# Optimization experiments

Measured on AMD Instinct MI355X. Metric: run time of the kernel, lower is better.

## Reference

```python
import jax, jax.numpy as jnp
import numpy as np

D = 1024          # node_vec_size = 16 heads * 64 head_size
HEADS = 16
DH = 64
HID = 4096        # TFM_HIDDEN_SIZE
L = 12            # TFM_NUM_LAYERS
NC = 256          # num concepts present (WMG2_MAX_CONCEPTS)
CSZ = 128         # WMG2_CONCEPT_SIZE
MAX_AGE = 256     # WMG2_MAX_AGE
AGE_V = MAX_AGE + 2  # 258
OBS = 2048
OUT = 512         # WMG2_OUTPUT_LAYER_SIZE
SCALE = 0.02


def setup_inputs() -> dict:
    key = jax.random.key(0)
    ks = iter(jax.random.split(key, 40))
    rn = lambda shape: jax.random.normal(next(ks), shape, dtype=jnp.float32) * SCALE
    inp = {
        'observation': jax.random.normal(next(ks), (OBS,), dtype=jnp.float32),
        'concepts': jax.random.normal(next(ks), (NC, CSZ), dtype=jnp.float32),
        'W_core': rn((D, OBS)), 'b_core': jnp.zeros((D,), jnp.float32),
        'W_cemb': rn((D, CSZ)), 'b_cemb': jnp.zeros((D,), jnp.float32),
        'W_age': rn((D, AGE_V)), 'b_age': jnp.zeros((D,), jnp.float32),
        'Wq': rn((L, D, D)), 'bq': jnp.zeros((L, D), jnp.float32),
        'Wk': rn((L, D, D)), 'bk': jnp.zeros((L, D), jnp.float32),
        'Wv': rn((L, D, D)), 'bv': jnp.zeros((L, D), jnp.float32),
        'Wo': rn((L, D, D)), 'bo': jnp.zeros((L, D), jnp.float32),
        'ln1_g': jnp.ones((L, D), jnp.float32), 'ln1_b': jnp.zeros((L, D), jnp.float32),
        'W1': rn((L, HID, D)), 'b1': jnp.zeros((L, HID), jnp.float32),
        'W2': rn((L, D, HID)), 'b2': jnp.zeros((L, D), jnp.float32),
        'ln2_g': jnp.ones((L, D), jnp.float32), 'ln2_b': jnp.zeros((L, D), jnp.float32),
        'W_concept': rn((CSZ, D)), 'b_concept': jnp.zeros((CSZ,), jnp.float32),
        'W_out': rn((OUT, D)), 'b_out': jnp.zeros((OUT,), jnp.float32),
    }
    return inp


def _layernorm(x, g, b, eps=1e-5):
    m = jnp.mean(x, axis=-1, keepdims=True)
    v = jnp.var(x, axis=-1, keepdims=True)
    return (x - m) * jax.lax.rsqrt(v + eps) * g + b


def _forward(observation, concepts, W_core, b_core, W_cemb, b_cemb, W_age, b_age,
             Wq, bq, Wk, bk, Wv, bv, Wo, bo, ln1_g, ln1_b, W1, b1, W2, b2,
             ln2_g, ln2_b, W_concept, b_concept, W_out, b_out):
    # --- embed observation node ---
    x0 = observation @ W_core.T + b_core                      # [D]
    # --- embed concept nodes, vectorized age embedding ---
    ages = jnp.arange(NC)
    oh = jax.nn.one_hot(jnp.minimum(ages, AGE_V - 1), AGE_V, dtype=jnp.float32)
    oh = oh.at[:, -1].set(ages.astype(jnp.float32) / MAX_AGE)  # age[-1] = age/MAX_AGE
    age_emb = oh @ W_age.T + b_age                             # [NC, D]
    xc = concepts @ W_cemb.T + b_cemb + age_emb                # [NC, D]
    x = jnp.concatenate([x0[None, :], xc], axis=0)             # [S, D], S = 1+NC

    # --- transformer (post-LN encoder), scan over layers ---
    def layer(h, p):
        wq, bq_, wk, bk_, wv, bv_, wo, bo_, g1, be1, w1, b1_, w2, b2_, g2, be2 = p
        S = h.shape[0]
        q = (h @ wq.T + bq_).reshape(S, HEADS, DH)
        k = (h @ wk.T + bk_).reshape(S, HEADS, DH)
        v = (h @ wv.T + bv_).reshape(S, HEADS, DH)
        scores = jnp.einsum('qhd,khd->hqk', q, k) / jnp.sqrt(jnp.float32(DH))
        attn = jax.nn.softmax(scores, axis=-1)
        o = jnp.einsum('hqk,khd->qhd', attn, v).reshape(S, D)
        h = _layernorm(h + (o @ wo.T + bo_), g1, be1)
        f = jax.nn.relu(h @ w1.T + b1_) @ w2.T + b2_
        h = _layernorm(h + f, g2, be2)
        return h, None

    x, _ = jax.lax.scan(layer, x, (Wq, bq, Wk, bk, Wv, bv, Wo, bo,
                                   ln1_g, ln1_b, W1, b1, W2, b2, ln2_g, ln2_b))
    tfm_out = x[0]                                             # [D] (node 0)
    new_concept = jnp.tanh(tfm_out @ W_concept.T + b_concept)  # [CSZ]
    output = jax.nn.relu(tfm_out @ W_out.T + b_out)[None, :]   # [1, OUT]
    return output, new_concept


def reference(observation, concepts, W_core, b_core, W_cemb, b_cemb, W_age, b_age,
              Wq, bq, Wk, bk, Wv, bv, Wo, bo, ln1_g, ln1_b, W1, b1, W2, b2,
              ln2_g, ln2_b, W_concept, b_concept, W_out, b_out):
    return _forward(observation, concepts, W_core, b_core, W_cemb, b_cemb, W_age, b_age,
                    Wq, bq, Wk, bk, Wv, bv, Wo, bo, ln1_g, ln1_b, W1, b1, W2, b2,
                    ln2_g, ln2_b, W_concept, b_concept, W_out, b_out)
```

## Files before the change

kernel.cpp:

```cpp
#include <hip/hip_runtime.h>
#include <hip/hip_bf16.h>
#include <cmath>

constexpr int D     = 1024;
constexpr int HEADS = 16;
constexpr int DH    = 64;
constexpr int HID   = 4096;
constexpr int NL    = 12;
constexpr int NC    = 256;
constexpr int CSZ   = 128;
constexpr int AGE_V = 258;
constexpr int OBS   = 2048;
constexpr int OUTN  = 512;
constexpr int S     = 257;
constexpr int SP    = 288;

typedef __attribute__((ext_vector_type(8))) short bf16x8v;
typedef __attribute__((ext_vector_type(4))) short short4v;
typedef __attribute__((ext_vector_type(4))) float f32x4;

__device__ __forceinline__ short bfc(float x) {
    __hip_bfloat16 h = __float2bfloat16(x);
    return __builtin_bit_cast(short, h);
}
__device__ __forceinline__ void st_bf16x4(short* p, float4 v) {
    short4v s;
    s.x = bfc(v.x); s.y = bfc(v.y); s.z = bfc(v.z); s.w = bfc(v.w);
    *(short4v*)p = s;
}

constexpr int BM = 96, BN = 32, BK = 64, LDT = 72;

template<int EPI>
__device__ __forceinline__ void gemm_core(const short* __restrict__ A,
                                          const float* __restrict__ B,
                                          const float* __restrict__ bias,
                                          void* __restrict__ Cp,
                                          int K, int N, int kbeg, int klen) {
    __shared__ __align__(16) short As[BM * LDT];
    __shared__ __align__(16) short Bs[BN * LDT];
    const int t  = threadIdx.x;
    const int m0 = blockIdx.y * BM;
    const int n0 = blockIdx.x * BN;
    const int ar = t >> 3;
    const int ac = (t & 7) * 8;
    const short* Ab = A + (size_t)(m0 + ar) * K + kbeg + ac;
    const int sr = t >> 4;
    const int sc = (t & 15) * 4;
    const float* Bb = B + (size_t)(n0 + sr) * K + kbeg + sc;

    const int lane = t & 63, wave = t >> 6;
    const int wm = wave >> 1, wn = wave & 1;
    const int fr = lane & 15, quad = lane >> 4;
    const short* Abase = &As[(wm * 48 + fr) * LDT + quad * 8];
    const short* Bbase = &Bs[(wn * 16 + fr) * LDT + quad * 8];

    f32x4 acc[3] = {};

    bf16x8v areg[3];
    float4  breg[2];
    #pragma unroll
    for (int p = 0; p < 3; ++p)
        areg[p] = *(const bf16x8v*)(Ab + (size_t)(p * 32) * K);
    #pragma unroll
    for (int p = 0; p < 2; ++p)
        breg[p] = *(const float4*)(Bb + (size_t)(p * 16) * K);

    for (int k0 = 0; k0 < klen; k0 += BK) {
        __syncthreads();
        #pragma unroll
        for (int p = 0; p < 3; ++p)
            *(bf16x8v*)&As[(p * 32 + ar) * LDT + ac] = areg[p];
        #pragma unroll
        for (int p = 0; p < 2; ++p)
            st_bf16x4(&Bs[(p * 16 + sr) * LDT + sc], breg[p]);
        __syncthreads();
        if (k0 + BK < klen) {
            #pragma unroll
            for (int p = 0; p < 3; ++p)
                areg[p] = *(const bf16x8v*)(Ab + (size_t)(p * 32) * K + (k0 + BK));
            #pragma unroll
            for (int p = 0; p < 2; ++p)
                breg[p] = *(const float4*)(Bb + (size_t)(p * 16) * K + (k0 + BK));
        }
        #pragma unroll
        for (int kt = 0; kt < 2; ++kt) {
            bf16x8v af[3], bf;
            #pragma unroll
            for (int mt = 0; mt < 3; ++mt)
                af[mt] = *(const bf16x8v*)(Abase + mt * 16 * LDT + kt * 32);
            bf = *(const bf16x8v*)(Bbase + kt * 32);
            #pragma unroll
            for (int mt = 0; mt < 3; ++mt)
                acc[mt] = __builtin_amdgcn_mfma_f32_16x16x32_bf16(
                    af[mt], bf, acc[mt], 0, 0, 0);
        }
    }

    #pragma unroll
    for (int mt = 0; mt < 3; ++mt) {
        const int m = m0 + wm * 48 + mt * 16 + quad * 4;
        const int n = n0 + wn * 16 + fr;
        if (EPI == 2) {
            float* C = (float*)Cp;
            #pragma unroll
            for (int r = 0; r < 4; ++r)
                atomicAdd(&C[(size_t)(m + r) * N + n], acc[mt][r]);
        } else if (EPI == 1) {
            short* C = (short*)Cp;
            const float bvv = bias[n];
            #pragma unroll
            for (int r = 0; r < 4; ++r)
                C[(size_t)(m + r) * N + n] = bfc(fmaxf(acc[mt][r] + bvv, 0.f));
        } else {
            float* C = (float*)Cp;
            const float bvv = bias[n];
            #pragma unroll
            for (int r = 0; r < 4; ++r)
                C[(size_t)(m + r) * N + n] = acc[mt][r] + bvv;
        }
    }
}

template<int EPI>
__global__ __launch_bounds__(256, 3)
void gemm_splitk(const short* __restrict__ A, const float* __restrict__ B,
                 const float* __restrict__ bias, void* __restrict__ C,
                 int K, int N, int klen) {
    gemm_core<EPI>(A, B, bias, C, K, N, blockIdx.z * klen, klen);
}

struct QKVArgs {
    const float* B[3];
    const float* bias[3];
    float* C[3];
};

__global__ __launch_bounds__(256, 3)
void gemm_qkv(const short* __restrict__ A, QKVArgs args, int K, int N) {
    const int z = blockIdx.z;
    gemm_core<0>(A, args.B[z], args.bias[z], args.C[z], K, N, 0, K);
}

constexpr int QB = 8, KT = 32, NT = 9;

__global__ __launch_bounds__(512)
void attn_kernel(const float* __restrict__ Q, const float* __restrict__ Km,
                 const float* __restrict__ V, short* __restrict__ O) {
    __shared__ float Ks[KT * 66];
    __shared__ float Vs[KT * 64];
    __shared__ float pw[QB][NT * KT];
    const int h = blockIdx.y;
    const int t = threadIdx.x;
    const int wq = t >> 6, lane = t & 63;
    const int q = blockIdx.x * QB + wq;
    const bool qok = q < S;
    const int k32 = lane & 31, dh2 = lane >> 5;

    float qr[32];
    #pragma unroll
    for (int i = 0; i < 32; ++i)
        qr[i] = qok ? Q[(size_t)q * D + h * DH + dh2 * 32 + i] : 0.f;

    float s[NT];
    for (int tile = 0; tile < NT; ++tile) {
        const int kk0 = tile * KT;
        __syncthreads();
        #pragma unroll
        for (int p = 0; p < 2; ++p) {
            const int idx = t + p * 512;
            const int kr = idx >> 5, c2 = (idx & 31) * 2;
            const int kg = kk0 + kr;
            float2 v = make_float2(0.f, 0.f);
            if (kg < S) v = *(const float2*)&Km[(size_t)kg * D + h * DH + c2];
            *(float2*)&Ks[kr * 66 + c2] = v;
        }
        __syncthreads();
        float dot = 0.f;
        const float* kp = &Ks[k32 * 66 + dh2 * 32];
        #pragma unroll
        for (int i = 0; i < 32; ++i) dot = fmaf(qr[i], kp[i], dot);
        dot += __shfl_xor(dot, 32, 64);
        s[tile] = (kk0 + k32 < S) ? dot * 0.125f : -1e30f;
    }
    float mx = -1e30f;
    #pragma unroll
    for (int j = 0; j < NT; ++j) mx = fmaxf(mx, s[j]);
    #pragma unroll
    for (int off = 32; off; off >>= 1) mx = fmaxf(mx, __shfl_xor(mx, off, 64));
    float sum = 0.f;
    #pragma unroll
    for (int j = 0; j < NT; ++j) {
        const float e = __expf(s[j] - mx);
        s[j] = e;
        sum += e;
    }
    #pragma unroll
    for (int off = 32; off; off >>= 1) sum += __shfl_xor(sum, off, 64);
    sum *= 0.5f;
    const float inv = 1.f / sum;
    if (qok && dh2 == 0) {
        #pragma unroll
        for (int j = 0; j < NT; ++j) pw[wq][j * KT + k32] = s[j] * inv;
    }
    float acc = 0.f;
    for (int tile = 0; tile < NT; ++tile) {
        const int kk0 = tile * KT;
        __syncthreads();
        {
            const int kr = t >> 4, c4 = (t & 15) * 4;
            const int kg = kk0 + kr;
            float4 v = make_float4(0.f, 0.f, 0.f, 0.f);
            if (kg < S) v = *(const float4*)&V[(size_t)kg * D + h * DH + c4];
            *(float4*)&Vs[kr * 64 + c4] = v;
        }
        __syncthreads();
        if (qok) {
            const float* pwp = &pw[wq][kk0];
            #pragma unroll
            for (int k = 0; k < KT; ++k)
                acc = fmaf(pwp[k], Vs[k * 64 + lane], acc);
        }
    }
    if (qok) O[(size_t)q * D + h * DH + lane] = bfc(acc);
}

__global__ __launch_bounds__(256)
void embed_obs_kernel(const float* __restrict__ obs, const float* __restrict__ Wc,
                      const float* __restrict__ bc, const float* __restrict__ bo0,
                      float* __restrict__ H, short* __restrict__ HB,
                      float* __restrict__ T) {
    const int d = blockIdx.x;
    const int t = threadIdx.x;
    const float4* w4 = (const float4*)&Wc[(size_t)d * OBS];
    const float4* o4 = (const float4*)obs;
    float acc = 0.f;
    #pragma unroll
    for (int i = t; i < OBS / 4; i += 256) {
        const float4 a = o4[i];
        const float4 b = w4[i];
        acc = fmaf(a.x, b.x, acc); acc = fmaf(a.y, b.y, acc);
        acc = fmaf(a.z, b.z, acc); acc = fmaf(a.w, b.w, acc);
    }
    __shared__ float red[256];
    red[t] = acc;
    __syncthreads();
    for (int off = 128; off; off >>= 1) {
        if (t < off) red[t] += red[t + off];
        __syncthreads();
    }
    if (t == 0) {
        const float v = red[0] + bc[d];
        H[d] = v;
        HB[d] = bfc(v);
        T[d] = v + bo0[d];
    }
}

__global__ __launch_bounds__(256)
void embed_concepts_kernel(const float* __restrict__ concepts, const float* __restrict__ Wce,
                           const float* __restrict__ bce, const float* __restrict__ Wa,
                           const float* __restrict__ ba, const float* __restrict__ bo0,
                           float* __restrict__ H, short* __restrict__ HB,
                           short* __restrict__ ATT, float* __restrict__ T) {
    const int row = blockIdx.x + 1;
    const int d = blockIdx.y * 256 + threadIdx.x;
    if (row > NC) {
        H[(size_t)row * D + d] = 0.f;
        HB[(size_t)row * D + d] = 0;
        ATT[(size_t)row * D + d] = 0;
        T[(size_t)row * D + d] = bo0[d];
        return;
    }
    const int i = row - 1;
    __shared__ __align__(16) float cs[CSZ];
    if (threadIdx.x < CSZ) cs[threadIdx.x] = concepts[(size_t)i * CSZ + threadIdx.x];
    __syncthreads();
    const float4* w4 = (const float4*)&Wce[(size_t)d * CSZ];
    const float4* c4 = (const float4*)cs;
    float acc = 0.f;
    #pragma unroll
    for (int c = 0; c < CSZ / 4; ++c) {
        const float4 a = c4[c];
        const float4 b = w4[c];
        acc = fmaf(a.x, b.x, acc); acc = fmaf(a.y, b.y, acc);
        acc = fmaf(a.z, b.z, acc); acc = fmaf(a.w, b.w, acc);
    }
    const float age = Wa[(size_t)d * AGE_V + i] +
                      ((float)i / 256.f) * Wa[(size_t)d * AGE_V + (AGE_V - 1)];
    const float v = acc + bce[d] + ba[d] + age;
    H[(size_t)row * D + d] = v;
    HB[(size_t)row * D + d] = bfc(v);
    T[(size_t)row * D + d] = v + bo0[d];
}

__global__ __launch_bounds__(256)
void ln_kernel(const float* __restrict__ X, const float* __restrict__ g,
               const float* __restrict__ b, float* __restrict__ Y,
               short* __restrict__ Yb,
               float* __restrict__ Tinit, const float* __restrict__ nbias) {
    const int r = blockIdx.x;
    const int t = threadIdx.x;
    const float* x = X + (size_t)r * D;
    float sm = 0.f, ss = 0.f;
    float v[4];
    #pragma unroll
    for (int j = 0; j < 4; ++j) {
        const float u = x[t + j * 256];
        v[j] = u;
        sm += u;
        ss = fmaf(u, u, ss);
    }
    __shared__ float r1[256], r2[256];
    r1[t] = sm; r2[t] = ss;
    __syncthreads();
    for (int off = 128; off; off >>= 1) {
        if (t < off) { r1[t] += r1[t + off]; r2[t] += r2[t + off]; }
        __syncthreads();
    }
    const float m   = r1[0] * (1.f / D);
    const float var = r2[0] * (1.f / D) - m * m;
    const float rs  = rsqrtf(var + 1e-5f);
    #pragma unroll
    for (int j = 0; j < 4; ++j) {
        const int idx = t + j * 256;
        const float y = (v[j] - m) * rs * g[idx] + b[idx];
        Y[(size_t)r * D + idx] = y;
        Yb[(size_t)r * D + idx] = bfc(y);
        if (Tinit) Tinit[(size_t)r * D + idx] = y + nbias[idx];
    }
}

__global__ __launch_bounds__(256)
void head_kernel(const float* __restrict__ H, const float* __restrict__ Wout,
                 const float* __restrict__ bout, const float* __restrict__ Wcon,
                 const float* __restrict__ bcon, float* __restrict__ out) {
    const int j = blockIdx.x;
    const int t = threadIdx.x;
    const float* w = (j < OUTN) ? &Wout[(size_t)j * D] : &Wcon[(size_t)(j - OUTN) * D];
    const float4* w4 = (const float4*)w;
    const float4* h4 = (const float4*)H;
    const float4 a = h4[t];
    const float4 b = w4[t];
    float acc = a.x * b.x + a.y * b.y + a.z * b.z + a.w * b.w;
    __shared__ float red[256];
    red[t] = acc;
    __syncthreads();
    for (int off = 128; off; off >>= 1) {
        if (t < off) red[t] += red[t + off];
        __syncthreads();
    }
    if (t == 0) {
        const float v = red[0] + ((j < OUTN) ? bout[j] : bcon[j - OUTN]);
        out[j] = (j < OUTN) ? fmaxf(v, 0.f) : tanhf(v);
    }
}

extern "C" void kernel_launch(void* const* d_in, const int* in_sizes, int n_in,
                              void* d_out, int out_size, void* d_ws, size_t ws_size,
                              hipStream_t stream) {
    (void)in_sizes; (void)n_in; (void)out_size; (void)ws_size;
    const float* obs     = (const float*)d_in[0];
    const float* concepts= (const float*)d_in[1];
    const float* W_core  = (const float*)d_in[2];
    const float* b_core  = (const float*)d_in[3];
    const float* W_cemb  = (const float*)d_in[4];
    const float* b_cemb  = (const float*)d_in[5];
    const float* W_age   = (const float*)d_in[6];
    const float* b_age   = (const float*)d_in[7];
    const float* Wq      = (const float*)d_in[8];
    const float* bq      = (const float*)d_in[9];
    const float* Wk      = (const float*)d_in[10];
    const float* bk      = (const float*)d_in[11];
    const float* Wv      = (const float*)d_in[12];
    const float* bv      = (const float*)d_in[13];
    const float* Wo      = (const float*)d_in[14];
    const float* bo      = (const float*)d_in[15];
    const float* ln1g    = (const float*)d_in[16];
    const float* ln1b    = (const float*)d_in[17];
    const float* W1      = (const float*)d_in[18];
    const float* b1      = (const float*)d_in[19];
    const float* W2      = (const float*)d_in[20];
    const float* b2      = (const float*)d_in[21];
    const float* ln2g    = (const float*)d_in[22];
    const float* ln2b    = (const float*)d_in[23];
    const float* W_con   = (const float*)d_in[24];
    const float* b_con   = (const float*)d_in[25];
    const float* W_out   = (const float*)d_in[26];
    const float* b_out   = (const float*)d_in[27];
    float* outp = (float*)d_out;

    float* ws   = (float*)d_ws;
    float* h    = ws;
    float* tmpA = h    + (size_t)SP * D;
    float* tmpB = tmpA + (size_t)SP * D;
    float* qb   = tmpB + (size_t)SP * D;
    float* kb   = qb   + (size_t)SP * D;
    float* vb   = kb   + (size_t)SP * D;
    short* hb   = (short*)(vb + (size_t)SP * D);
    short* att  = hb  + (size_t)SP * D;
    short* mid  = att + (size_t)SP * D;

    embed_obs_kernel<<<dim3(D), 256, 0, stream>>>(obs, W_core, b_core, bo, h, hb, tmpA);
    embed_concepts_kernel<<<dim3(SP - 1, D / 256), 256, 0, stream>>>(
        concepts, W_cemb, b_cemb, W_age, b_age, bo, h, hb, att, tmpA);

    for (int l = 0; l < NL; ++l) {
        QKVArgs qa;
        qa.B[0] = Wq + (size_t)l * D * D;  qa.bias[0] = bq + (size_t)l * D;  qa.C[0] = qb;
        qa.B[1] = Wk + (size_t)l * D * D;  qa.bias[1] = bk + (size_t)l * D;  qa.C[1] = kb;
        qa.B[2] = Wv + (size_t)l * D * D;  qa.bias[2] = bv + (size_t)l * D;  qa.C[2] = vb;
        gemm_qkv<<<dim3(D / BN, SP / BM, 3), 256, 0, stream>>>(hb, qa, D, D);
        attn_kernel<<<dim3((S + QB - 1) / QB, HEADS), 512, 0, stream>>>(qb, kb, vb, att);
        gemm_splitk<2><<<dim3(D / BN, SP / BM, 4), 256, 0, stream>>>(
            att, Wo + (size_t)l * D * D, nullptr, tmpA, D, D, 256);
        ln_kernel<<<dim3(S), 256, 0, stream>>>(tmpA, ln1g + (size_t)l * D,
                                               ln1b + (size_t)l * D, h, hb,
                                               tmpB, b2 + (size_t)l * D);
        gemm_splitk<1><<<dim3(HID / BN, SP / BM, 1), 256, 0, stream>>>(
            hb, W1 + (size_t)l * HID * D, b1 + (size_t)l * HID, mid, D, HID, D);
        gemm_splitk<2><<<dim3(D / BN, SP / BM, 8), 256, 0, stream>>>(
            mid, W2 + (size_t)l * D * HID, nullptr, tmpB, HID, D, 512);
        float* ti = (l + 1 < NL) ? tmpA : nullptr;
        const float* nb = (l + 1 < NL) ? (bo + (size_t)(l + 1) * D) : nullptr;
        ln_kernel<<<dim3(S), 256, 0, stream>>>(tmpB, ln2g + (size_t)l * D,
                                               ln2b + (size_t)l * D, h, hb, ti, nb);
    }
    head_kernel<<<dim3(OUTN + CSZ), 256, 0, stream>>>(h, W_out, b_out, W_con, b_con, outp);
}
```

Before: 1.541 ms.

## Fuse whole transformer forward into one cooperative persistent megakernel with grid syncs

Replaces the sequence of roughly a hundred separate kernel launches with a single cooperative persistent kernel. Each stage (embeddings, QKV GEMM, attention, output projection, layernorms, FFN GEMMs, head) becomes a device job loop over a grid-stride schedule, separated by grid.sync, and all stages share one static shared-memory buffer. This is meant to remove per-launch overhead and inter-kernel gaps. Attention is re-tiled to 4 queries per 256-thread block, and the W2 split-K factor drops from 8 to 4 inside the megakernel. The trade-offs are grid-wide barrier costs, fewer blocks per GEMM stage, and register limits from the shared launch bounds. A non-cooperative multi-launch fallback is kept for when the cooperative launch fails.

```diff
diff --git a/kernel.cpp b/kernel.cpp
--- a/kernel.cpp
+++ b/kernel.cpp
@@ -1,6 +1,9 @@
 #include <hip/hip_runtime.h>
+#include <hip/hip_cooperative_groups.h>
 #include <hip/hip_bf16.h>
 #include <cmath>
+
+namespace cg = cooperative_groups;
 
 constexpr int D     = 1024;
 constexpr int HEADS = 16;
@@ -30,24 +33,23 @@
 }
 
 constexpr int BM = 96, BN = 32, BK = 64, LDT = 72;
+constexpr int SMEM_BYTES = 21504;
 
 template<int EPI>
-__device__ __forceinline__ void gemm_core(const short* __restrict__ A,
-                                          const float* __restrict__ B,
-                                          const float* __restrict__ bias,
-                                          void* __restrict__ Cp,
-                                          int K, int N, int kbeg, int klen) {
-    __shared__ __align__(16) short As[BM * LDT];
-    __shared__ __align__(16) short Bs[BN * LDT];
-    const int t  = threadIdx.x;
-    const int m0 = blockIdx.y * BM;
-    const int n0 = blockIdx.x * BN;
+__device__ __forceinline__ void gemm_job(char* smraw, const short* __restrict__ A,
+                                         const float* __restrict__ Bm,
+                                         const float* __restrict__ bias,
+                                         void* __restrict__ Cp,
+                                         int K, int N, int kbeg, int klen,
+                                         int m0, int n0, int t) {
+    short* As = (short*)smraw;
+    short* Bs = (short*)(smraw + 13824);
     const int ar = t >> 3;
     const int ac = (t & 7) * 8;
     const short* Ab = A + (size_t)(m0 + ar) * K + kbeg + ac;
     const int sr = t >> 4;
     const int sc = (t & 15) * 4;
-    const float* Bb = B + (size_t)(n0 + sr) * K + kbeg + sc;
+    const float* Bb = Bm + (size_t)(n0 + sr) * K + kbeg + sc;
 
     const int lane = t & 63, wave = t >> 6;
     const int wm = wave >> 1, wn = wave & 1;
@@ -56,7 +58,6 @@
     const short* Bbase = &Bs[(wn * 16 + fr) * LDT + quad * 8];
 
     f32x4 acc[3] = {};
-
     bf16x8v areg[3];
     float4  breg[2];
     #pragma unroll
@@ -85,15 +86,15 @@
         }
         #pragma unroll
         for (int kt = 0; kt < 2; ++kt) {
-            bf16x8v af[3], bf;
+            bf16x8v af[3], bfv;
             #pragma unroll
             for (int mt = 0; mt < 3; ++mt)
                 af[mt] = *(const bf16x8v*)(Abase + mt * 16 * LDT + kt * 32);
-            bf = *(const bf16x8v*)(Bbase + kt * 32);
+            bfv = *(const bf16x8v*)(Bbase + kt * 32);
             #pragma unroll
             for (int mt = 0; mt < 3; ++mt)
                 acc[mt] = __builtin_amdgcn_mfma_f32_16x16x32_bf16(
-                    af[mt], bf, acc[mt], 0, 0, 0);
+                    af[mt], bfv, acc[mt], 0, 0, 0);
         }
     }
 
@@ -122,38 +123,18 @@
     }
 }
 
-template<int EPI>
-__global__ __launch_bounds__(256, 3)
-void gemm_splitk(const short* __restrict__ A, const float* __restrict__ B,
-                 const float* __restrict__ bias, void* __restrict__ C,
-                 int K, int N, int klen) {
-    gemm_core<EPI>(A, B, bias, C, K, N, blockIdx.z * klen, klen);
-}
-
-struct QKVArgs {
-    const float* B[3];
-    const float* bias[3];
-    float* C[3];
-};
-
-__global__ __launch_bounds__(256, 3)
-void gemm_qkv(const short* __restrict__ A, QKVArgs args, int K, int N) {
-    const int z = blockIdx.z;
-    gemm_core<0>(A, args.B[z], args.bias[z], args.C[z], K, N, 0, K);
-}
-
-constexpr int QB = 8, KT = 32, NT = 9;
-
-__global__ __launch_bounds__(512)
-void attn_kernel(const float* __restrict__ Q, const float* __restrict__ Km,
-                 const float* __restrict__ V, short* __restrict__ O) {
-    __shared__ float Ks[KT * 66];
-    __shared__ float Vs[KT * 64];
-    __shared__ float pw[QB][NT * KT];
-    const int h = blockIdx.y;
-    const int t = threadIdx.x;
+constexpr int KT = 32, NT = 9;
+
+__device__ __forceinline__ void attn_job(char* smraw, const float* __restrict__ Q,
+                                         const float* __restrict__ Km,
+                                         const float* __restrict__ V,
+                                         short* __restrict__ O,
+                                         int h, int qt, int t) {
+    float* Ks = (float*)smraw;
+    float* Vs = (float*)(smraw + 8448);
+    float* pw = (float*)(smraw + 8448 + 8192);
     const int wq = t >> 6, lane = t & 63;
-    const int q = blockIdx.x * QB + wq;
+    const int q = qt * 4 + wq;
     const bool qok = q < S;
     const int k32 = lane & 31, dh2 = lane >> 5;
 
@@ -167,8 +148,8 @@
         const int kk0 = tile * KT;
         __syncthreads();
         #pragma unroll
-        for (int p = 0; p < 2; ++p) {
-            const int idx = t + p * 512;
+        for (int p = 0; p < 4; ++p) {
+            const int idx = t + p * 256;
             const int kr = idx >> 5, c2 = (idx & 31) * 2;
             const int kg = kk0 + kr;
             float2 v = make_float2(0.f, 0.f);
@@ -201,14 +182,16 @@
     const float inv = 1.f / sum;
     if (qok && dh2 == 0) {
         #pragma unroll
-        for (int j = 0; j < NT; ++j) pw[wq][j * KT + k32] = s[j] * inv;
+        for (int j = 0; j < NT; ++j) pw[wq * 288 + j * KT + k32] = s[j] * inv;
     }
     float acc = 0.f;
     for (int tile = 0; tile < NT; ++tile) {
         const int kk0 = tile * KT;
         __syncthreads();
-        {
-            const int kr = t >> 4, c4 = (t & 15) * 4;
+        #pragma unroll
+        for (int p = 0; p < 2; ++p) {
+            const int idx = t + p * 256;
+            const int kr = idx >> 4, c4 = (idx & 15) * 4;
             const int kg = kk0 + kr;
             float4 v = make_float4(0.f, 0.f, 0.f, 0.f);
             if (kg < S) v = *(const float4*)&V[(size_t)kg * D + h * DH + c4];
@@ -216,7 +199,7 @@
         }
         __syncthreads();
         if (qok) {
-            const float* pwp = &pw[wq][kk0];
+            const float* pwp = &pw[wq * 288 + kk0];
             #pragma unroll
             for (int k = 0; k < KT; ++k)
                 acc = fmaf(pwp[k], Vs[k * 64 + lane], acc);
@@ -225,13 +208,13 @@
     if (qok) O[(size_t)q * D + h * DH + lane] = bfc(acc);
 }
 
-__global__ __launch_bounds__(256)
-void embed_obs_kernel(const float* __restrict__ obs, const float* __restrict__ Wc,
-                      const float* __restrict__ bc, const float* __restrict__ bo0,
-                      float* __restrict__ H, short* __restrict__ HB,
-                      float* __restrict__ T) {
-    const int d = blockIdx.x;
-    const int t = threadIdx.x;
+__device__ __forceinline__ void embed_obs_job(char* smraw, const float* __restrict__ obs,
+                                              const float* __restrict__ Wc,
+                                              const float* __restrict__ bc,
+                                              const float* __restrict__ bo0,
+                                              float* __restrict__ H, short* __restrict__ HB,
+                                              float* __restrict__ T, int d, int t) {
+    float* red = (float*)smraw;
     const float4* w4 = (const float4*)&Wc[(size_t)d * OBS];
     const float4* o4 = (const float4*)obs;
     float acc = 0.f;
@@ -242,7 +225,7 @@
         acc = fmaf(a.x, b.x, acc); acc = fmaf(a.y, b.y, acc);
         acc = fmaf(a.z, b.z, acc); acc = fmaf(a.w, b.w, acc);
     }
-    __shared__ float red[256];
+    __syncthreads();
     red[t] = acc;
     __syncthreads();
     for (int off = 128; off; off >>= 1) {
@@ -257,14 +240,17 @@
     }
 }
 
-__global__ __launch_bounds__(256)
-void embed_concepts_kernel(const float* __restrict__ concepts, const float* __restrict__ Wce,
-                           const float* __restrict__ bce, const float* __restrict__ Wa,
-                           const float* __restrict__ ba, const float* __restrict__ bo0,
-                           float* __restrict__ H, short* __restrict__ HB,
-                           short* __restrict__ ATT, float* __restrict__ T) {
-    const int row = blockIdx.x + 1;
-    const int d = blockIdx.y * 256 + threadIdx.x;
+__device__ __forceinline__ void embed_cpt_job(char* smraw, const float* __restrict__ concepts,
+                                              const float* __restrict__ Wce,
+                                              const float* __restrict__ bce,
+                                              const float* __restrict__ Wa,
+                                              const float* __restrict__ ba,
+                                              const float* __restrict__ bo0,
+                                              float* __restrict__ H, short* __restrict__ HB,
+                                              short* __restrict__ ATT, float* __restrict__ T,
+                                              int j, int t) {
+    const int row = (j % 287) + 1;
+    const int d = (j / 287) * 256 + t;
     if (row > NC) {
         H[(size_t)row * D + d] = 0.f;
         HB[(size_t)row * D + d] = 0;
@@ -272,9 +258,10 @@
         T[(size_t)row * D + d] = bo0[d];
         return;
     }
+    float* cs = (float*)smraw;
     const int i = row - 1;
-    __shared__ __align__(16) float cs[CSZ];
-    if (threadIdx.x < CSZ) cs[threadIdx.x] = concepts[(size_t)i * CSZ + threadIdx.x];
+    __syncthreads();
+    if (t < CSZ) cs[t] = concepts[(size_t)i * CSZ + t];
     __syncthreads();
     const float4* w4 = (const float4*)&Wce[(size_t)d * CSZ];
     const float4* c4 = (const float4*)cs;
@@ -294,13 +281,13 @@
     T[(size_t)row * D + d] = v + bo0[d];
 }
 
-__global__ __launch_bounds__(256)
-void ln_kernel(const float* __restrict__ X, const float* __restrict__ g,
-               const float* __restrict__ b, float* __restrict__ Y,
-               short* __restrict__ Yb,
-               float* __restrict__ Tinit, const float* __restrict__ nbias) {
-    const int r = blockIdx.x;
-    const int t = threadIdx.x;
+__device__ __forceinline__ void ln_job(char* smraw, const float* __restrict__ X,
+                                       const float* __restrict__ g, const float* __restrict__ b,
+                                       float* __restrict__ Y, short* __restrict__ Yb,
+                                       float* __restrict__ Ti, const float* __restrict__ nbias,
+                                       int r, int t) {
+    float* r1 = (float*)smraw;
+    float* r2 = r1 + 256;
     const float* x = X + (size_t)r * D;
     float sm = 0.f, ss = 0.f;
     float v[4];
@@ -311,7 +298,7 @@
         sm += u;
         ss = fmaf(u, u, ss);
     }
-    __shared__ float r1[256], r2[256];
+    __syncthreads();
     r1[t] = sm; r2[t] = ss;
     __syncthreads();
     for (int off = 128; off; off >>= 1) {
@@ -327,23 +314,24 @@
         const float y = (v[j] - m) * rs * g[idx] + b[idx];
         Y[(size_t)r * D + idx] = y;
         Yb[(size_t)r * D + idx] = bfc(y);
-        if (Tinit) Tinit[(size_t)r * D + idx] = y + nbias[idx];
-    }
-}
-
-__global__ __launch_bounds__(256)
-void head_kernel(const float* __restrict__ H, const float* __restrict__ Wout,
-                 const float* __restrict__ bout, const float* __restrict__ Wcon,
-                 const float* __restrict__ bcon, float* __restrict__ out) {
-    const int j = blockIdx.x;
-    const int t = threadIdx.x;
+        if (Ti) Ti[(size_t)r * D + idx] = y + nbias[idx];
+    }
+}
+
+__device__ __forceinline__ void head_job(char* smraw, const float* __restrict__ H,
+                                         const float* __restrict__ Wout,
+                                         const float* __restrict__ bout,
+                                         const float* __restrict__ Wcon,
+                                         const float* __restrict__ bcon,
+                                         float* __restrict__ out, int j, int t) {
+    float* red = (float*)smraw;
     const float* w = (j < OUTN) ? &Wout[(size_t)j * D] : &Wcon[(size_t)(j - OUTN) * D];
     const float4* w4 = (const float4*)w;
     const float4* h4 = (const float4*)H;
     const float4 a = h4[t];
     const float4 b = w4[t];
     float acc = a.x * b.x + a.y * b.y + a.z * b.z + a.w * b.w;
-    __shared__ float red[256];
+    __syncthreads();
     red[t] = acc;
     __syncthreads();
     for (int off = 128; off; off >>= 1) {
@@ -354,6 +342,117 @@
         const float v = red[0] + ((j < OUTN) ? bout[j] : bcon[j - OUTN]);
         out[j] = (j < OUTN) ? fmaxf(v, 0.f) : tanhf(v);
     }
+}
+
+struct MP {
+    const float *obs, *concepts, *W_core, *b_core, *W_cemb, *b_cemb, *W_age, *b_age;
+    const float *Wq, *bq, *Wk, *bk, *Wv, *bv, *Wo, *bo;
+    const float *ln1g, *ln1b, *W1, *b1, *W2, *b2, *ln2g, *ln2b;
+    const float *W_con, *b_con, *W_out, *b_out;
+    float *outp;
+    float *h, *tmpA, *tmpB, *qb, *kb, *vb;
+    short *hb, *att, *mid;
+};
+
+__global__ __launch_bounds__(256, 2)
+void mega(MP p) {
+    __shared__ __align__(16) char smraw[SMEM_BYTES];
+    cg::grid_group grid = cg::this_grid();
+    const int t = threadIdx.x;
+    const int nb = gridDim.x, bid = blockIdx.x;
+
+    for (int j = bid; j < D; j += nb)
+        embed_obs_job(smraw, p.obs, p.W_core, p.b_core, p.bo, p.h, p.hb, p.tmpA, j, t);
+    for (int j = bid; j < 287 * 4; j += nb)
+        embed_cpt_job(smraw, p.concepts, p.W_cemb, p.b_cemb, p.W_age, p.b_age, p.bo,
+                      p.h, p.hb, p.att, p.tmpA, j, t);
+    grid.sync();
+
+    for (int l = 0; l < NL; ++l) {
+        const size_t lo = (size_t)l * D * D;
+        for (int j = bid; j < 288; j += nb) {
+            const int n = j & 31, m = (j >> 5) % 3, z = j / 96;
+            const float *Bm, *bs;
+            float* Cm;
+            if (z == 0)      { Bm = p.Wq + lo; bs = p.bq + (size_t)l * D; Cm = p.qb; }
+            else if (z == 1) { Bm = p.Wk + lo; bs = p.bk + (size_t)l * D; Cm = p.kb; }
+            else             { Bm = p.Wv + lo; bs = p.bv + (size_t)l * D; Cm = p.vb; }
+            gemm_job<0>(smraw, p.hb, Bm, bs, Cm, D, D, 0, D, m * 96, n * 32, t);
+        }
+        grid.sync();
+        for (int j = bid; j < 65 * 16; j += nb)
+            attn_job(smraw, p.qb, p.kb, p.vb, p.att, j / 65, j % 65, t);
+        grid.sync();
+        for (int j = bid; j < 384; j += nb) {
+            const int n = j & 31, m = (j >> 5) % 3, z = j / 96;
+            gemm_job<2>(smraw, p.att, p.Wo + lo, nullptr, p.tmpA, D, D,
+                        z * 256, 256, m * 96, n * 32, t);
+        }
+        grid.sync();
+        for (int j = bid; j < S; j += nb)
+            ln_job(smraw, p.tmpA, p.ln1g + (size_t)l * D, p.ln1b + (size_t)l * D,
+                   p.h, p.hb, p.tmpB, p.b2 + (size_t)l * D, j, t);
+        grid.sync();
+        for (int j = bid; j < 384; j += nb) {
+            const int n = j % 128, m = j / 128;
+            gemm_job<1>(smraw, p.hb, p.W1 + (size_t)l * HID * D, p.b1 + (size_t)l * HID,
+                        p.mid, D, HID, 0, D, m * 96, n * 32, t);
+        }
+        grid.sync();
+        for (int j = bid; j < 384; j += nb) {
+            const int n = j & 31, m = (j >> 5) % 3, z = j / 96;
+            gemm_job<2>(smraw, p.mid, p.W2 + (size_t)l * D * HID, nullptr, p.tmpB,
+                        HID, D, z * 1024, 1024, m * 96, n * 32, t);
+        }
+        grid.sync();
+        float* ti = (l + 1 < NL) ? p.tmpA : nullptr;
+        const float* nbias = (l + 1 < NL) ? p.bo + (size_t)(l + 1) * D : nullptr;
+        for (int j = bid; j < S; j += nb)
+            ln_job(smraw, p.tmpB, p.ln2g + (size_t)l * D, p.ln2b + (size_t)l * D,
+                   p.h, p.hb, ti, nbias, j, t);
+        grid.sync();
+    }
+    for (int j = bid; j < OUTN + CSZ; j += nb)
+        head_job(smraw, p.h, p.W_out, p.b_out, p.W_con, p.b_con, p.outp, j, t);
+}
+
+template<int EPI>
+__global__ __launch_bounds__(256, 3)
+void k_gemm(const short* __restrict__ A, const float* __restrict__ Bm,
+            const float* __restrict__ bias, void* __restrict__ C,
+            int K, int N, int klen) {
+    __shared__ __align__(16) char sm[18432];
+    gemm_job<EPI>(sm, A, Bm, bias, C, K, N, blockIdx.z * klen, klen,
+                  blockIdx.y * BM, blockIdx.x * BN, threadIdx.x);
+}
+__global__ __launch_bounds__(256)
+void k_attn(const float* Q, const float* Km, const float* V, short* O) {
+    __shared__ __align__(16) char sm[21248];
+    attn_job(sm, Q, Km, V, O, blockIdx.y, blockIdx.x, threadIdx.x);
+}
+__global__ __launch_bounds__(256)
+void k_ln(const float* X, const float* g, const float* b, float* Y, short* Yb,
+          float* Ti, const float* nb) {
+    __shared__ __align__(16) char sm[2048];
+    ln_job(sm, X, g, b, Y, Yb, Ti, nb, blockIdx.x, threadIdx.x);
+}
+__global__ __launch_bounds__(256)
+void k_eobs(const float* obs, const float* Wc, const float* bc, const float* bo0,
+            float* H, short* HB, float* T) {
+    __shared__ __align__(16) char sm[1024];
+    embed_obs_job(sm, obs, Wc, bc, bo0, H, HB, T, blockIdx.x, threadIdx.x);
+}
+__global__ __launch_bounds__(256)
+void k_ecpt(const float* c, const float* Wce, const float* bce, const float* Wa,
+            const float* ba, const float* bo0, float* H, short* HB, short* ATT, float* T) {
+    __shared__ __align__(16) char sm[512];
+    embed_cpt_job(sm, c, Wce, bce, Wa, ba, bo0, H, HB, ATT, T, blockIdx.x, threadIdx.x);
+}
+__global__ __launch_bounds__(256)
+void k_head(const float* H, const float* Wout, const float* bout, const float* Wcon,
+            const float* bcon, float* out) {
+    __shared__ __align__(16) char sm[1024];
+    head_job(sm, H, Wout, bout, Wcon, bcon, out, blockIdx.x, threadIdx.x);
 }
 
 extern "C" void kernel_launch(void* const* d_in, const int* in_sizes, int n_in,
@@ -401,30 +500,50 @@
     short* att  = hb  + (size_t)SP * D;
     short* mid  = att + (size_t)SP * D;
 
-    embed_obs_kernel<<<dim3(D), 256, 0, stream>>>(obs, W_core, b_core, bo, h, hb, tmpA);
-    embed_concepts_kernel<<<dim3(SP - 1, D / 256), 256, 0, stream>>>(
-        concepts, W_cemb, b_cemb, W_age, b_age, bo, h, hb, att, tmpA);
-
-    for (int l = 0; l < NL; ++l) {
-        QKVArgs qa;
-        qa.B[0] = Wq + (size_t)l * D * D;  qa.bias[0] = bq + (size_t)l * D;  qa.C[0] = qb;
-        qa.B[1] = Wk + (size_t)l * D * D;  qa.bias[1] = bk + (size_t)l * D;  qa.C[1] = kb;
-        qa.B[2] = Wv + (size_t)l * D * D;  qa.bias[2] = bv + (size_t)l * D;  qa.C[2] = vb;
-        gemm_qkv<<<dim3(D / BN, SP / BM, 3), 256, 0, stream>>>(hb, qa, D, D);
-        attn_kernel<<<dim3((S + QB - 1) / QB, HEADS), 512, 0, stream>>>(qb, kb, vb, att);
-        gemm_splitk<2><<<dim3(D / BN, SP / BM, 4), 256, 0, stream>>>(
-            att, Wo + (size_t)l * D * D, nullptr, tmpA, D, D, 256);
-        ln_kernel<<<dim3(S), 256, 0, stream>>>(tmpA, ln1g + (size_t)l * D,
-                                               ln1b + (size_t)l * D, h, hb,
-                                               tmpB, b2 + (size_t)l * D);
-        gemm_splitk<1><<<dim3(HID / BN, SP / BM, 1), 256, 0, stream>>>(
-            hb, W1 + (size_t)l * HID * D, b1 + (size_t)l * HID, mid, D, HID, D);
-        gemm_splitk<2><<<dim3(D / BN, SP / BM, 8), 256, 0, stream>>>(
-            mid, W2 + (size_t)l * D * HID, nullptr, tmpB, HID, D, 512);
-        float* ti = (l + 1 < NL) ? tmpA : nullptr;
-        const float* nb = (l + 1 < NL) ? (bo + (size_t)(l + 1) * D) : nullptr;
-        ln_kernel<<<dim3(S), 256, 0, stream>>>(tmpB, ln2g + (size_t)l * D,
-                                               ln2b + (size_t)l * D, h, hb, ti, nb);
-    }
-    head_kernel<<<dim3(OUTN + CSZ), 256, 0, stream>>>(h, W_out, b_out, W_con, b_con, outp);
-}
+    MP p;
+    p.obs = obs; p.concepts = concepts; p.W_core = W_core; p.b_core = b_core;
+    p.W_cemb = W_cemb; p.b_cemb = b_cemb; p.W_age = W_age; p.b_age = b_age;
+    p.Wq = Wq; p.bq = bq; p.Wk = Wk; p.bk = bk; p.Wv = Wv; p.bv = bv;
+    p.Wo = Wo; p.bo = bo; p.ln1g = ln1g; p.ln1b = ln1b; p.W1 = W1; p.b1 = b1;
+    p.W2 = W2; p.b2 = b2; p.ln2g = ln2g; p.ln2b = ln2b;
+    p.W_con = W_con; p.b_con = b_con; p.W_out = W_out; p.b_out = b_out;
+    p.outp = outp;
+    p.h = h; p.tmpA = tmpA; p.tmpB = tmpB; p.qb = qb; p.kb = kb; p.vb = vb;
+    p.hb = hb; p.att = att; p.mid = mid;
+
+    static int g_grid = 0;
+    if (g_grid == 0) {
+        int mb = 0;
+        if (hipOccupancyMaxActiveBlocksPerMultiprocessor(&mb, mega, 256, 0) != hipSuccess
+            || mb < 1) mb = 1;
+        if (mb > 2) mb = 2;
+        g_grid = 256 * mb;
+    }
+    void* kp[1] = { (void*)&p };
+    hipError_t e = hipLaunchCooperativeKernel(mega, dim3(g_grid), dim3(256), kp, 0u, stream);
+    if (e != hipSuccess) {
+        (void)hipGetLastError();
+        k_eobs<<<dim3(D), 256, 0, stream>>>(obs, W_core, b_core, bo, h, hb, tmpA);
+        k_ecpt<<<dim3(287 * 4), 256, 0, stream>>>(concepts, W_cemb, b_cemb, W_age,
+                                                  b_age, bo, h, hb, att, tmpA);
+        for (int l = 0; l < NL; ++l) {
+            const size_t lo = (size_t)l * D * D;
+            k_gemm<0><<<dim3(32, 3, 1), 256, 0, stream>>>(hb, Wq + lo, bq + (size_t)l * D, qb, D, D, D);
+            k_gemm<0><<<dim3(32, 3, 1), 256, 0, stream>>>(hb, Wk + lo, bk + (size_t)l * D, kb, D, D, D);
+            k_gemm<0><<<dim3(32, 3, 1), 256, 0, stream>>>(hb, Wv + lo, bv + (size_t)l * D, vb, D, D, D);
+            k_attn<<<dim3(65, 16), 256, 0, stream>>>(qb, kb, vb, att);
+            k_gemm<2><<<dim3(32, 3, 4), 256, 0, stream>>>(att, Wo + lo, nullptr, tmpA, D, D, 256);
+            k_ln<<<dim3(S), 256, 0, stream>>>(tmpA, ln1g + (size_t)l * D, ln1b + (size_t)l * D,
+                                              h, hb, tmpB, b2 + (size_t)l * D);
+            k_gemm<1><<<dim3(128, 3, 1), 256, 0, stream>>>(hb, W1 + (size_t)l * HID * D,
+                                                           b1 + (size_t)l * HID, mid, D, HID, D);
+            k_gemm<2><<<dim3(32, 3, 8), 256, 0, stream>>>(mid, W2 + (size_t)l * D * HID,
+                                                          nullptr, tmpB, HID, D, 512);
+            float* ti = (l + 1 < NL) ? tmpA : nullptr;
+            const float* nb2 = (l + 1 < NL) ? (bo + (size_t)(l + 1) * D) : nullptr;
+            k_ln<<<dim3(S), 256, 0, stream>>>(tmpB, ln2g + (size_t)l * D, ln2b + (size_t)l * D,
+                                              h, hb, ti, nb2);
+        }
+        k_head<<<dim3(OUTN + CSZ), 256, 0, stream>>>(h, W_out, b_out, W_con, b_con, outp);
+    }
+}
```

New measurement: 5.133 ms. 3.33x slower.
